# Kernel optimization log

Hardware: AMD Instinct MI355X
Metric: run time of the kernel (lower is better)

## Reference

```python
import jax, jax.numpy as jnp
import numpy as np
from jax import lax

T = 32768
INPUT = 1024
HIDDEN = 1024
OUTPUT = 1024


def setup_inputs() -> dict:
    key = jax.random.key(0)
    k1, k2, k3, k4, k5 = jax.random.split(key, 5)
    return {
        "x": jax.random.normal(k1, (1, T, INPUT), dtype=jnp.float32),
        "W_i2h": jax.random.normal(k2, (HIDDEN, INPUT + HIDDEN), dtype=jnp.float32) * 0.02,
        "b_i2h": jax.random.normal(k3, (HIDDEN,), dtype=jnp.float32) * 0.02,
        "W_h2o": jax.random.normal(k4, (OUTPUT, HIDDEN), dtype=jnp.float32) * 0.02,
        "b_h2o": jax.random.normal(k5, (OUTPUT,), dtype=jnp.float32) * 0.02,
    }


def reference(x, W_i2h, b_i2h, W_h2o, b_h2o):
    # x: [1, T, input]; original iterates timesteps of x[0] with batch-1 state.
    seq = x[0]  # [T, input]
    h0 = jnp.zeros((1, HIDDEN), dtype=x.dtype)

    # Split i2h weight so we avoid a per-step concat: [hidden, input+hidden]
    W_x = W_i2h[:, :INPUT]   # acts on token
    W_h = W_i2h[:, INPUT:]   # acts on hidden

    def step(h, x_t):
        # h: [1, hidden], x_t: [input]
        h_new = jnp.tanh(x_t[None, :] @ W_x.T + h @ W_h.T + b_i2h)
        return h_new, None

    h_T, _ = lax.scan(step, h0, seq)
    # Original computes h2o every step but returns only the last output.
    output = h_T @ W_h2o.T + b_h2o  # [1, output]
    return output
```

## Files before the change

kernel.cpp:

```cpp
#include <hip/hip_runtime.h>

#define T_STEPS 32768
#define HID 1024
#define NWG 64
#define PRE_BYTES ((size_t)T_STEPS * HID * 2)
#define HP_BYTES  (2 * HID * 8)

typedef float vf4 __attribute__((ext_vector_type(4)));
typedef unsigned long long u64;

__device__ __forceinline__ unsigned short f2bf(float f) {
    unsigned u = __float_as_uint(f);
    u = (u + 0x7fffu + ((u >> 16) & 1u)) >> 16;
    return (unsigned short)u;
}
__device__ __forceinline__ float bf2f(unsigned short s) {
    return __uint_as_float(((unsigned)s) << 16);
}

#define BM 64
#define BN 64
#define BK 16
#define LDST 68

__global__ void __launch_bounds__(256) pre_gemm(
    const float* __restrict__ x, const float* __restrict__ Wi,
    const float* __restrict__ b, unsigned short* __restrict__ pre)
{
    __shared__ float As[BK * LDST];
    __shared__ float Bs[BK * LDST];
    const int tid = threadIdx.x;
    const int t0 = blockIdx.x * BM;
    const int j0 = blockIdx.y * BN;
    const int row = tid >> 2;
    const int kq  = tid & 3;
    const int tx  = tid & 15;
    const int ty  = tid >> 4;

    float c[4][4];
#pragma unroll
    for (int i = 0; i < 4; ++i)
#pragma unroll
        for (int j = 0; j < 4; ++j) c[i][j] = 0.f;

    for (int k0 = 0; k0 < 1024; k0 += BK) {
        float4 a4 = *(const float4*)&x[(size_t)(t0 + row) * 1024 + k0 + 4 * kq];
        float4 b4 = *(const float4*)&Wi[(size_t)(j0 + row) * 2048 + k0 + 4 * kq];
        __syncthreads();
        As[(4 * kq + 0) * LDST + row] = a4.x;
        As[(4 * kq + 1) * LDST + row] = a4.y;
        As[(4 * kq + 2) * LDST + row] = a4.z;
        As[(4 * kq + 3) * LDST + row] = a4.w;
        Bs[(4 * kq + 0) * LDST + row] = b4.x;
        Bs[(4 * kq + 1) * LDST + row] = b4.y;
        Bs[(4 * kq + 2) * LDST + row] = b4.z;
        Bs[(4 * kq + 3) * LDST + row] = b4.w;
        __syncthreads();
#pragma unroll
        for (int kk = 0; kk < BK; ++kk) {
            float4 av = *(const float4*)&As[kk * LDST + 4 * ty];
            float4 bv = *(const float4*)&Bs[kk * LDST + 4 * tx];
            c[0][0] = fmaf(av.x, bv.x, c[0][0]); c[0][1] = fmaf(av.x, bv.y, c[0][1]);
            c[0][2] = fmaf(av.x, bv.z, c[0][2]); c[0][3] = fmaf(av.x, bv.w, c[0][3]);
            c[1][0] = fmaf(av.y, bv.x, c[1][0]); c[1][1] = fmaf(av.y, bv.y, c[1][1]);
            c[1][2] = fmaf(av.y, bv.z, c[1][2]); c[1][3] = fmaf(av.y, bv.w, c[1][3]);
            c[2][0] = fmaf(av.z, bv.x, c[2][0]); c[2][1] = fmaf(av.z, bv.y, c[2][1]);
            c[2][2] = fmaf(av.z, bv.z, c[2][2]); c[2][3] = fmaf(av.z, bv.w, c[2][3]);
            c[3][0] = fmaf(av.w, bv.x, c[3][0]); c[3][1] = fmaf(av.w, bv.y, c[3][1]);
            c[3][2] = fmaf(av.w, bv.z, c[3][2]); c[3][3] = fmaf(av.w, bv.w, c[3][3]);
        }
    }

    float4 bias = *(const float4*)&b[j0 + 4 * tx];
#pragma unroll
    for (int i = 0; i < 4; ++i) {
        int r = t0 + 4 * ty + i;
        ushort4 u;
        u.x = f2bf(c[i][0] + bias.x);
        u.y = f2bf(c[i][1] + bias.y);
        u.z = f2bf(c[i][2] + bias.z);
        u.w = f2bf(c[i][3] + bias.w);
        *(ushort4*)&pre[(size_t)r * 1024 + j0 + 4 * tx] = u;
    }
}

__device__ __forceinline__ vf4 ldg4_pin(const float* p) {
    vf4 r;
    asm volatile("global_load_dwordx4 %0, %1, off\n\ts_waitcnt vmcnt(0)"
                 : "=v"(r) : "v"(p) : "memory");
    return r;
}
__device__ __forceinline__ u64 pack_hv(float v, unsigned t) {
    return ((u64)t << 32) | (u64)__float_as_uint(v);
}
__device__ __forceinline__ float fast_tanh(float x) {
    float a = fabsf(x);
    float e = __expf(a + a);
    float r = 1.f - 2.f * __builtin_amdgcn_rcpf(e + 1.f);
    return copysignf(r, x);
}

__global__ void __launch_bounds__(1024, 4) rnn_rec(
    const unsigned short* __restrict__ pre,
    const float* __restrict__ Wi,
    const float* __restrict__ Wo,
    const float* __restrict__ bo,
    float* __restrict__ out,
    u64* hp)
{
    const int tid = threadIdx.x;
    const int w   = tid >> 6;
    const int l   = tid & 63;
    const int r   = blockIdx.x * 16 + w;

    __shared__ __align__(16) float hl[2][HID];
    __shared__ int s_abort;
    if (tid == 0) s_abort = 0;

    vf4 wv0, wv1, wv2, wv3;
    {
        const float* wp = Wi + (size_t)r * 2048 + 1024 + 16 * l;
        wv0 = ldg4_pin(wp + 0);
        wv1 = ldg4_pin(wp + 4);
        wv2 = ldg4_pin(wp + 8);
        wv3 = ldg4_pin(wp + 12);
    }
    __syncthreads();

    int budget = 4000000;

    for (int t = 1; t <= T_STEPS; ++t) {
        const int par = (t - 1) & 1;

        float prev = 0.f;
        if (l == 0) prev = bf2f(pre[(size_t)(t - 1) * HID + r]);

        {
            const u64* src = hp + (size_t)par * HID + tid;
            const unsigned tg = (unsigned)(t - 1);
            u64 q;
            for (;;) {
                q = __hip_atomic_load(src, __ATOMIC_RELAXED, __HIP_MEMORY_SCOPE_AGENT);
                if ((unsigned)(q >> 32) == tg) break;
                if (--budget < 0) { s_abort = 1; break; }
            }
            hl[par][tid] = __uint_as_float((unsigned)q);
        }
        __syncthreads();
        if (s_abort) return;

        const float* hb = &hl[par][16 * l];
        vf4 a0 = *(const vf4*)&hb[0];
        vf4 a1 = *(const vf4*)&hb[4];
        vf4 a2 = *(const vf4*)&hb[8];
        vf4 a3 = *(const vf4*)&hb[12];
        float acc0 = 0.f, acc1 = 0.f;
        acc0 = fmaf(wv0.x, a0.x, acc0); acc0 = fmaf(wv0.y, a0.y, acc0);
        acc0 = fmaf(wv0.z, a0.z, acc0); acc0 = fmaf(wv0.w, a0.w, acc0);
        acc1 = fmaf(wv1.x, a1.x, acc1); acc1 = fmaf(wv1.y, a1.y, acc1);
        acc1 = fmaf(wv1.z, a1.z, acc1); acc1 = fmaf(wv1.w, a1.w, acc1);
        acc0 = fmaf(wv2.x, a2.x, acc0); acc0 = fmaf(wv2.y, a2.y, acc0);
        acc0 = fmaf(wv2.z, a2.z, acc0); acc0 = fmaf(wv2.w, a2.w, acc0);
        acc1 = fmaf(wv3.x, a3.x, acc1); acc1 = fmaf(wv3.y, a3.y, acc1);
        acc1 = fmaf(wv3.z, a3.z, acc1); acc1 = fmaf(wv3.w, a3.w, acc1);
        float s = acc0 + acc1;
        s += __shfl_xor(s, 1);
        s += __shfl_xor(s, 2);
        s += __shfl_xor(s, 4);
        s += __shfl_xor(s, 8);
        s += __shfl_xor(s, 16);
        s += __shfl_xor(s, 32);

        if (l == 0) {
            float h = fast_tanh(prev + s);
            __hip_atomic_store(&hp[(size_t)(t & 1) * HID + r], pack_hv(h, (unsigned)t),
                               __ATOMIC_RELAXED, __HIP_MEMORY_SCOPE_AGENT);
        }
    }

    {
        const int par = T_STEPS & 1;
        const u64* src = hp + (size_t)par * HID + tid;
        const unsigned tg = (unsigned)T_STEPS;
        u64 q;
        for (;;) {
            q = __hip_atomic_load(src, __ATOMIC_RELAXED, __HIP_MEMORY_SCOPE_AGENT);
            if ((unsigned)(q >> 32) == tg) break;
            if (--budget < 0) { s_abort = 1; break; }
        }
        hl[0][tid] = __uint_as_float((unsigned)q);
        __syncthreads();
        if (s_abort) return;

        const float* hb = &hl[0][16 * l];
        const float* wo = Wo + (size_t)r * 1024 + 16 * l;
        vf4 a0 = *(const vf4*)&hb[0];
        vf4 a1 = *(const vf4*)&hb[4];
        vf4 a2 = *(const vf4*)&hb[8];
        vf4 a3 = *(const vf4*)&hb[12];
        vf4 w0 = *(const vf4*)&wo[0];
        vf4 w1 = *(const vf4*)&wo[4];
        vf4 w2 = *(const vf4*)&wo[8];
        vf4 w3 = *(const vf4*)&wo[12];
        float acc0 = 0.f, acc1 = 0.f;
        acc0 = fmaf(w0.x, a0.x, acc0); acc0 = fmaf(w0.y, a0.y, acc0);
        acc0 = fmaf(w0.z, a0.z, acc0); acc0 = fmaf(w0.w, a0.w, acc0);
        acc1 = fmaf(w1.x, a1.x, acc1); acc1 = fmaf(w1.y, a1.y, acc1);
        acc1 = fmaf(w1.z, a1.z, acc1); acc1 = fmaf(w1.w, a1.w, acc1);
        acc0 = fmaf(w2.x, a2.x, acc0); acc0 = fmaf(w2.y, a2.y, acc0);
        acc0 = fmaf(w2.z, a2.z, acc0); acc0 = fmaf(w2.w, a2.w, acc0);
        acc1 = fmaf(w3.x, a3.x, acc1); acc1 = fmaf(w3.y, a3.y, acc1);
        acc1 = fmaf(w3.z, a3.z, acc1); acc1 = fmaf(w3.w, a3.w, acc1);
        float s = acc0 + acc1;
        s += __shfl_xor(s, 1);
        s += __shfl_xor(s, 2);
        s += __shfl_xor(s, 4);
        s += __shfl_xor(s, 8);
        s += __shfl_xor(s, 16);
        s += __shfl_xor(s, 32);
        if (l == 0) out[r] = s + bo[r];
    }
}

extern "C" void kernel_launch(void* const* d_in, const int* in_sizes, int n_in,
                              void* d_out, int out_size, void* d_ws, size_t ws_size,
                              hipStream_t stream) {
    const float* x     = (const float*)d_in[0];
    const float* W_i2h = (const float*)d_in[1];
    const float* b_i2h = (const float*)d_in[2];
    const float* W_h2o = (const float*)d_in[3];
    const float* b_h2o = (const float*)d_in[4];
    float* out = (float*)d_out;

    char* base = (char*)d_ws;
    unsigned short* pre = (unsigned short*)base;
    u64* hp = (u64*)(base + PRE_BYTES);

    hipMemsetAsync(hp, 0, HP_BYTES, stream);
    pre_gemm<<<dim3(T_STEPS / BM, HID / BN), 256, 0, stream>>>(x, W_i2h, b_i2h, pre);
    rnn_rec<<<NWG, 1024, 0, stream>>>(pre, W_i2h, W_h2o, b_h2o, out, hp);
}
```

Baseline: 64.71 ms.

## Spread recurrence over 128 smaller workgroups with padded hidden-state slots

The recurrent kernel now runs 128 workgroups of 512 threads, each handling 8 hidden rows instead of 16, so each thread polls two hidden values per step. Each published hidden value gets its own 64-byte slot (MBS padding), which separates the flags that workgroups poll on. Weight and hidden-vector access is changed to a strided 4*l pattern so LDS reads spread across banks. Doubling the number of workgroups in the grid-wide spin barrier may raise synchronisation latency and L2 polling traffic per step.

```diff
diff --git a/kernel.cpp b/kernel.cpp
--- a/kernel.cpp
+++ b/kernel.cpp
@@ -2,9 +2,11 @@
 
 #define T_STEPS 32768
 #define HID 1024
-#define NWG 64
+#define NWG 128
+#define RPW 8
+#define MBS 8
 #define PRE_BYTES ((size_t)T_STEPS * HID * 2)
-#define HP_BYTES  (2 * HID * 8)
+#define HP_BYTES  (2 * HID * MBS * 8)
 
 typedef float vf4 __attribute__((ext_vector_type(4)));
 typedef unsigned long long u64;
@@ -100,7 +102,7 @@
     return copysignf(r, x);
 }
 
-__global__ void __launch_bounds__(1024, 4) rnn_rec(
+__global__ void __launch_bounds__(512, 2) rnn_rec(
     const unsigned short* __restrict__ pre,
     const float* __restrict__ Wi,
     const float* __restrict__ Wo,
@@ -111,7 +113,7 @@
     const int tid = threadIdx.x;
     const int w   = tid >> 6;
     const int l   = tid & 63;
-    const int r   = blockIdx.x * 16 + w;
+    const int r   = blockIdx.x * RPW + w;
 
     __shared__ __align__(16) float hl[2][HID];
     __shared__ int s_abort;
@@ -119,15 +121,16 @@
 
     vf4 wv0, wv1, wv2, wv3;
     {
-        const float* wp = Wi + (size_t)r * 2048 + 1024 + 16 * l;
+        const float* wp = Wi + (size_t)r * 2048 + 1024 + 4 * l;
         wv0 = ldg4_pin(wp + 0);
-        wv1 = ldg4_pin(wp + 4);
-        wv2 = ldg4_pin(wp + 8);
-        wv3 = ldg4_pin(wp + 12);
+        wv1 = ldg4_pin(wp + 256);
+        wv2 = ldg4_pin(wp + 512);
+        wv3 = ldg4_pin(wp + 768);
     }
     __syncthreads();
 
-    int budget = 4000000;
+    int budget = 8000000;
+    const int e0 = 2 * tid, e1 = 2 * tid + 1;
 
     for (int t = 1; t <= T_STEPS; ++t) {
         const int par = (t - 1) & 1;
@@ -136,24 +139,29 @@
         if (l == 0) prev = bf2f(pre[(size_t)(t - 1) * HID + r]);
 
         {
-            const u64* src = hp + (size_t)par * HID + tid;
+            const u64* s0 = hp + (size_t)par * (HID * MBS) + (size_t)e0 * MBS;
+            const u64* s1 = hp + (size_t)par * (HID * MBS) + (size_t)e1 * MBS;
             const unsigned tg = (unsigned)(t - 1);
-            u64 q;
+            u64 q0, q1;
             for (;;) {
-                q = __hip_atomic_load(src, __ATOMIC_RELAXED, __HIP_MEMORY_SCOPE_AGENT);
-                if ((unsigned)(q >> 32) == tg) break;
+                q0 = __hip_atomic_load(s0, __ATOMIC_RELAXED, __HIP_MEMORY_SCOPE_AGENT);
+                q1 = __hip_atomic_load(s1, __ATOMIC_RELAXED, __HIP_MEMORY_SCOPE_AGENT);
+                if (((unsigned)(q0 >> 32) == tg) & ((unsigned)(q1 >> 32) == tg)) break;
                 if (--budget < 0) { s_abort = 1; break; }
             }
-            hl[par][tid] = __uint_as_float((unsigned)q);
+            float2 v;
+            v.x = __uint_as_float((unsigned)q0);
+            v.y = __uint_as_float((unsigned)q1);
+            *(float2*)&hl[par][e0] = v;
         }
         __syncthreads();
         if (s_abort) return;
 
-        const float* hb = &hl[par][16 * l];
-        vf4 a0 = *(const vf4*)&hb[0];
-        vf4 a1 = *(const vf4*)&hb[4];
-        vf4 a2 = *(const vf4*)&hb[8];
-        vf4 a3 = *(const vf4*)&hb[12];
+        const float* hb = hl[par];
+        vf4 a0 = *(const vf4*)&hb[4 * l + 0];
+        vf4 a1 = *(const vf4*)&hb[4 * l + 256];
+        vf4 a2 = *(const vf4*)&hb[4 * l + 512];
+        vf4 a3 = *(const vf4*)&hb[4 * l + 768];
         float acc0 = 0.f, acc1 = 0.f;
         acc0 = fmaf(wv0.x, a0.x, acc0); acc0 = fmaf(wv0.y, a0.y, acc0);
         acc0 = fmaf(wv0.z, a0.z, acc0); acc0 = fmaf(wv0.w, a0.w, acc0);
@@ -173,35 +181,41 @@
 
         if (l == 0) {
             float h = fast_tanh(prev + s);
-            __hip_atomic_store(&hp[(size_t)(t & 1) * HID + r], pack_hv(h, (unsigned)t),
+            __hip_atomic_store(&hp[(size_t)(t & 1) * (HID * MBS) + (size_t)r * MBS],
+                               pack_hv(h, (unsigned)t),
                                __ATOMIC_RELAXED, __HIP_MEMORY_SCOPE_AGENT);
         }
     }
 
     {
         const int par = T_STEPS & 1;
-        const u64* src = hp + (size_t)par * HID + tid;
+        const u64* s0 = hp + (size_t)par * (HID * MBS) + (size_t)e0 * MBS;
+        const u64* s1 = hp + (size_t)par * (HID * MBS) + (size_t)e1 * MBS;
         const unsigned tg = (unsigned)T_STEPS;
-        u64 q;
+        u64 q0, q1;
         for (;;) {
-            q = __hip_atomic_load(src, __ATOMIC_RELAXED, __HIP_MEMORY_SCOPE_AGENT);
-            if ((unsigned)(q >> 32) == tg) break;
+            q0 = __hip_atomic_load(s0, __ATOMIC_RELAXED, __HIP_MEMORY_SCOPE_AGENT);
+            q1 = __hip_atomic_load(s1, __ATOMIC_RELAXED, __HIP_MEMORY_SCOPE_AGENT);
+            if (((unsigned)(q0 >> 32) == tg) & ((unsigned)(q1 >> 32) == tg)) break;
             if (--budget < 0) { s_abort = 1; break; }
         }
-        hl[0][tid] = __uint_as_float((unsigned)q);
+        float2 v;
+        v.x = __uint_as_float((unsigned)q0);
+        v.y = __uint_as_float((unsigned)q1);
+        *(float2*)&hl[0][e0] = v;
         __syncthreads();
         if (s_abort) return;
 
-        const float* hb = &hl[0][16 * l];
-        const float* wo = Wo + (size_t)r * 1024 + 16 * l;
-        vf4 a0 = *(const vf4*)&hb[0];
-        vf4 a1 = *(const vf4*)&hb[4];
-        vf4 a2 = *(const vf4*)&hb[8];
-        vf4 a3 = *(const vf4*)&hb[12];
+        const float* hb = hl[0];
+        const float* wo = Wo + (size_t)r * 1024 + 4 * l;
+        vf4 a0 = *(const vf4*)&hb[4 * l + 0];
+        vf4 a1 = *(const vf4*)&hb[4 * l + 256];
+        vf4 a2 = *(const vf4*)&hb[4 * l + 512];
+        vf4 a3 = *(const vf4*)&hb[4 * l + 768];
         vf4 w0 = *(const vf4*)&wo[0];
-        vf4 w1 = *(const vf4*)&wo[4];
-        vf4 w2 = *(const vf4*)&wo[8];
-        vf4 w3 = *(const vf4*)&wo[12];
+        vf4 w1 = *(const vf4*)&wo[256];
+        vf4 w2 = *(const vf4*)&wo[512];
+        vf4 w3 = *(const vf4*)&wo[768];
         float acc0 = 0.f, acc1 = 0.f;
         acc0 = fmaf(w0.x, a0.x, acc0); acc0 = fmaf(w0.y, a0.y, acc0);
         acc0 = fmaf(w0.z, a0.z, acc0); acc0 = fmaf(w0.w, a0.w, acc0);
@@ -238,5 +252,5 @@
 
     hipMemsetAsync(hp, 0, HP_BYTES, stream);
     pre_gemm<<<dim3(T_STEPS / BM, HID / BN), 256, 0, stream>>>(x, W_i2h, b_i2h, pre);
-    rnn_rec<<<NWG, 1024, 0, stream>>>(pre, W_i2h, W_h2o, b_h2o, out, hp);
-}
+    rnn_rec<<<NWG, 512, 0, stream>>>(pre, W_i2h, W_h2o, b_h2o, out, hp);
+}
```

Measured after the change: 63.74 ms. Within noise of the previous version (-1.5%).
